# Kernel tuning notes

Measured on AMD Instinct MI355X. Metric: run time of the kernel, lower is better.

Reference implementation:

```python
import jax, jax.numpy as jnp
import numpy as np
from jax import lax

DT = 0.01        # self.dt
DT_SCALE = 1.0   # forward default


def _christoffel(v, x, U, W):
    # Low-rank quadratic Christoffel contraction (U, W as in verlet_fused):
    # gamma = (tanh(x @ U) * (v @ U)^2) @ W        [B, D]
    h = v @ U                 # [B, R]
    gate = jnp.tanh(x @ U)    # [B, R]
    return (gate * h * h) @ W


def setup_inputs() -> dict:
    key = jax.random.key(0)
    ks = jax.random.split(key, 5)
    B, D, R = 4096, 1024, 256
    x = jax.random.normal(ks[0], (B, D), dtype=jnp.float32)
    v = jax.random.normal(ks[1], (B, D), dtype=jnp.float32)
    force = jax.random.normal(ks[2], (B, D), dtype=jnp.float32)
    U = jax.random.normal(ks[3], (D, R), dtype=jnp.float32) * (D ** -0.5)
    W = jax.random.normal(ks[4], (R, D), dtype=jnp.float32) * (R ** -0.5)
    return {"x": x, "v": v, "force": force, "U": U, "W": W, "steps": 8}


def reference(x, v, force, U, W, steps):
    dt = jnp.float32(DT * DT_SCALE)
    half = jnp.float32(0.5)

    def step(carry, _):
        x, v = carry
        a = force - _christoffel(v, x, U, W)
        v_half = v + half * dt * a
        x = x + dt * v_half
        a_next = force - _christoffel(v_half, x, U, W)
        v = v_half + half * dt * a_next
        return (x, v), None

    (x, v), _ = lax.scan(step, (x, v), None, length=steps)
    return (x, v)
```

## Files before the change

kernel.cpp:

```cpp
#include <hip/hip_runtime.h>

typedef __bf16 bf16_t;
typedef __bf16 bf16x2 __attribute__((ext_vector_type(2)));
typedef __bf16 bf16x8 __attribute__((ext_vector_type(8)));
typedef float f32x4 __attribute__((ext_vector_type(4)));

#define MFMA_BF16(a, b, c) __builtin_amdgcn_mfma_f32_16x16x32_bf16((a), (b), (c), 0, 0, 0)

static constexpr int Bn = 4096;
static constexpr int Dn = 1024;
static constexpr int Rn = 256;
static constexpr int BT = 16;
static constexpr float DTv = 0.01f;
static constexpr float HDT = 0.005f;

__device__ __forceinline__ int swz(int col) { return col ^ (((col >> 5) & 7) << 2); }

__global__ __launch_bounds__(1024)
void setup_kernel(const float* __restrict__ U, const float* __restrict__ W,
                  bf16_t* __restrict__ Upk, bf16_t* __restrict__ Wpk,
                  bf16_t* __restrict__ WUpk) {
  __shared__ __align__(16) bf16_t wbuf[16 * 1032];
  const int tid = (int)threadIdx.x;
  const int b = (int)blockIdx.x;
  if (b < 32) {
    int t = b * 1024 + tid;
    int l = t & 63, f = t >> 6;
    int kb = f & 31, ct = f >> 5;
    int row0 = kb * 32 + (l >> 4) * 8, col = ct * 16 + (l & 15);
    bf16x8 v;
#pragma unroll
    for (int j = 0; j < 8; ++j) v[j] = (bf16_t)U[(size_t)(row0 + j) * Rn + col];
    ((bf16x8*)Upk)[t] = v;
  } else if (b < 64) {
    int t = (b - 32) * 1024 + tid;
    int l = t & 63, f = t >> 6;
    int kb = f & 7, ct = f >> 3;
    int row0 = kb * 32 + (l >> 4) * 8, col = ct * 16 + (l & 15);
    bf16x8 v;
#pragma unroll
    for (int j = 0; j < 8; ++j) v[j] = (bf16_t)W[(size_t)(row0 + j) * Dn + col];
    ((bf16x8*)Wpk)[t] = v;
  } else {
    const int m = b - 64;
    const int wv = tid >> 6;
    const int l = tid & 63;
    const int ln = l & 15;
    const int quad = l >> 4;
    {
      int row = tid >> 6;
      int c0 = (tid & 63) * 16;
      const float* src = W + (size_t)(m * 16 + row) * Dn + c0;
      bf16_t* dst = wbuf + row * 1032 + c0;
#pragma unroll
      for (int j = 0; j < 16; ++j) dst[j] = (bf16_t)src[j];
    }
    __syncthreads();
    const int ucol = wv * 16 + ln;
    float uf[8][8];
#pragma unroll
    for (int p = 0; p < 8; ++p)
#pragma unroll
      for (int j = 0; j < 8; ++j)
        uf[p][j] = U[(size_t)(p * 32 + quad * 8 + j) * Rn + ucol];
    f32x4 acc = {0.f, 0.f, 0.f, 0.f};
    const bf16_t* arow = wbuf + ln * 1032 + quad * 8;
#pragma unroll
    for (int kb = 0; kb < 32; ++kb) {
      bf16x8 bb;
#pragma unroll
      for (int j = 0; j < 8; ++j) bb[j] = (bf16_t)uf[kb & 7][j];
      const bf16x8 a = *(const bf16x8*)(arow + kb * 32);
      acc = MFMA_BF16(a, bb, acc);
      if (kb < 24) {
#pragma unroll
        for (int j = 0; j < 8; ++j)
          uf[kb & 7][j] = U[(size_t)((kb + 8) * 32 + quad * 8 + j) * Rn + ucol];
      }
    }
#pragma unroll
    for (int r = 0; r < 4; ++r) {
      int rw = m * 16 + quad * 4 + r;
      int kb = rw >> 5;
      int sub = (rw >> 3) & 3;
      int j = rw & 7;
      size_t slot = ((size_t)(wv * 8 + kb) * 64 + sub * 16 + ln) * 8 + j;
      WUpk[slot] = (bf16_t)acc[r];
    }
  }
}

__global__ __launch_bounds__(1024)
__attribute__((amdgpu_waves_per_eu(4, 4)))
void integrate_kernel(const float* __restrict__ x_in, const float* __restrict__ v_in,
                      const float* __restrict__ force,
                      const bf16_t* __restrict__ Upk, const bf16_t* __restrict__ Wpk,
                      const bf16_t* __restrict__ WUpk,
                      const int* __restrict__ steps_p, float* __restrict__ out) {
  __shared__ __align__(16) char smem[49920];
  bf16_t* abuf = (bf16_t*)smem;
  float* fsb = (float*)smem;

  const int tid = (int)threadIdx.x;
  const int wv = tid >> 6;
  const int l = tid & 63;
  const int ln = l & 15;
  const int quad = l >> 4;
  const int s = steps_p[0];
  const int nhalf = 2 * s;
  const int row_base = (int)blockIdx.x * BT;

  float* out_x = out;
  float* out_v = out + (size_t)Bn * Dn;

  const int frow = tid >> 7;
  const int fr = (tid & 127) * 8;
  const int sc0 = swz(fr);
  const int sc1 = sc0 ^ 4;
  int csw[4];
#pragma unroll
  for (int i = 0; i < 4; ++i) csw[i] = swz((wv * 4 + i) * 16 + ln);

  float xs[4][4], vs[4][4];
  bf16x2 fs2[4][2];

  auto load_chunk = [&](const float* __restrict__ srcA, int HF, auto sink) {
    const float* src_ = srcA + (size_t)(row_base + HF * 8) * Dn;
    f32x4 a_ = *(const f32x4*)(src_ + tid * 8);
    f32x4 b_ = *(const f32x4*)(src_ + tid * 8 + 4);
    *(f32x4*)(fsb + frow * 1024 + sc0) = a_;
    *(f32x4*)(fsb + frow * 1024 + sc1) = b_;
    __syncthreads();
    if ((quad >> 1) == HF) {
#pragma unroll
      for (int i = 0; i < 4; ++i)
#pragma unroll
        for (int r = 0; r < 4; ++r)
          sink(i, r, fsb[((quad & 1) * 4 + r) * 1024 + csw[i]]);
    }
    __syncthreads();
  };
  load_chunk(x_in, 0, [&](int i, int r, float v_) { xs[i][r] = v_; });
  load_chunk(x_in, 1, [&](int i, int r, float v_) { xs[i][r] = v_; });
  load_chunk(v_in, 0, [&](int i, int r, float v_) { vs[i][r] = v_; });
  load_chunk(v_in, 1, [&](int i, int r, float v_) { vs[i][r] = v_; });
  load_chunk(force, 0, [&](int i, int r, float v_) { fs2[i][r >> 1][r & 1] = (bf16_t)v_; });
  load_chunk(force, 1, [&](int i, int r, float v_) { fs2[i][r >> 1][r & 1] = (bf16_t)v_; });

  f32x4 hx = {0.f, 0.f, 0.f, 0.f};
  f32x4 hv = {0.f, 0.f, 0.f, 0.f};
  f32x4 FU = {0.f, 0.f, 0.f, 0.f};
#pragma unroll
  for (int kh = 0; kh < 2; ++kh) {
    if ((wv >> 3) == kh) {
#pragma unroll
      for (int i = 0; i < 4; ++i) {
        const int col = (wv * 4 + i) * 16 + ln - kh * 512;
#pragma unroll
        for (int r = 0; r < 4; ++r) {
          const int ro = (quad * 4 + r) * 520 + col;
          abuf[ro] = (bf16_t)xs[i][r];
          abuf[8320 + ro] = (bf16_t)vs[i][r];
          abuf[16640 + ro] = fs2[i][r >> 1][r & 1];
        }
      }
    }
    __syncthreads();
    const bf16x8* up = (const bf16x8*)Upk + ((size_t)wv * 32 + kh * 16) * 64 + l;
    const bf16_t* ax = abuf + ln * 520 + quad * 8;
    bf16x8 ur[8];
#pragma unroll
    for (int p = 0; p < 8; ++p) ur[p] = up[p * 64];
#pragma unroll
    for (int kb = 0; kb < 16; ++kb) {
      const bf16x8 b = ur[kb & 7];
      if (kb < 8) ur[kb & 7] = up[(kb + 8) * 64];
      const bf16x8 a0 = *(const bf16x8*)(ax + kb * 32);
      const bf16x8 a1 = *(const bf16x8*)(ax + 8320 + kb * 32);
      const bf16x8 a2 = *(const bf16x8*)(ax + 16640 + kb * 32);
      hx = MFMA_BF16(a0, b, hx);
      hv = MFMA_BF16(a1, b, hv);
      FU = MFMA_BF16(a2, b, FU);
    }
    __syncthreads();
  }

  bf16x8 wu[8];
  {
    const bf16x8* wub = (const bf16x8*)WUpk + (size_t)wv * 8 * 64 + l;
#pragma unroll
    for (int kb = 0; kb < 8; ++kb) wu[kb] = wub[kb * 64];
  }

  f32x4 S1 = {0.f, 0.f, 0.f, 0.f};
  f32x4 S2 = {0.f, 0.f, 0.f, 0.f};
  bf16_t* tbase = (bf16_t*)smem;
  for (int h = 0; h < nhalf; ++h) {
    if (h & 1) {
#pragma unroll
      for (int r = 0; r < 4; ++r) hx[r] += DTv * hv[r];
    }
    const float ch = (float)(s - ((h + 1) >> 1));
    bf16_t* tb = tbase + (h & 1) * 4224;
#pragma unroll
    for (int r = 0; r < 4; ++r) {
      float a = fminf(fmaxf(hx[r], -15.f), 15.f);
      const float e = __expf(2.f * a);
      const float gate = (e - 1.f) / (e + 1.f);
      const float t = gate * hv[r] * hv[r];
      S1[r] += t;
      S2[r] += ch * t;
      tb[(quad * 4 + r) * 264 + wv * 16 + ln] = (bf16_t)t;
    }
    __syncthreads();
    f32x4 g0 = {0.f, 0.f, 0.f, 0.f};
    f32x4 g1 = {0.f, 0.f, 0.f, 0.f};
    const bf16_t* trow = tb + ln * 264 + quad * 8;
#pragma unroll
    for (int kb = 0; kb < 8; kb += 2) {
      g0 = MFMA_BF16(*(const bf16x8*)(trow + kb * 32), wu[kb], g0);
      g1 = MFMA_BF16(*(const bf16x8*)(trow + (kb + 1) * 32), wu[kb + 1], g1);
    }
#pragma unroll
    for (int r = 0; r < 4; ++r) hv[r] += HDT * (FU[r] - (g0[r] + g1[r]));
  }
  __syncthreads();

  bf16_t* sbuf = (bf16_t*)smem;
#pragma unroll
  for (int r = 0; r < 4; ++r) {
    const int ro = (quad * 4 + r) * 264 + wv * 16 + ln;
    sbuf[ro] = (bf16_t)S1[r];
    sbuf[4224 + ro] = (bf16_t)S2[r];
  }
  __syncthreads();
  f32x4 ac1[4], ac2[4];
#pragma unroll
  for (int i = 0; i < 4; ++i) {
    ac1[i] = (f32x4){0.f, 0.f, 0.f, 0.f};
    ac2[i] = (f32x4){0.f, 0.f, 0.f, 0.f};
  }
  {
    const bf16x8* wp = (const bf16x8*)Wpk + (size_t)(wv * 4) * 8 * 64 + l;
    const bf16_t* s1row = sbuf + ln * 264 + quad * 8;
    const bf16_t* s2row = s1row + 4224;
    bf16x8 wr[4];
#pragma unroll
    for (int i = 0; i < 4; ++i) wr[i] = wp[i * 8 * 64];
#pragma unroll
    for (int kb = 0; kb < 8; ++kb) {
      const bf16x8 a1 = *(const bf16x8*)(s1row + kb * 32);
      const bf16x8 a2 = *(const bf16x8*)(s2row + kb * 32);
#pragma unroll
      for (int i = 0; i < 4; ++i) {
        const bf16x8 b = wr[i];
        if (kb < 7) wr[i] = wp[i * 8 * 64 + (kb + 1) * 64];
        ac1[i] = MFMA_BF16(a1, b, ac1[i]);
        ac2[i] = MFMA_BF16(a2, b, ac2[i]);
      }
    }
  }
  __syncthreads();

  const float sf = (float)s;
  const float c_vf = sf * DTv;
  const float c_xf = sf * sf * DTv * HDT;
  auto store_chunk = [&](float* __restrict__ dstA, int HF, auto vex) {
    if ((quad >> 1) == HF) {
#pragma unroll
      for (int i = 0; i < 4; ++i)
#pragma unroll
        for (int r = 0; r < 4; ++r)
          fsb[((quad & 1) * 4 + r) * 1024 + csw[i]] = vex(i, r);
    }
    __syncthreads();
    float* dst_ = dstA + (size_t)(row_base + HF * 8) * Dn;
    *(f32x4*)(dst_ + tid * 8) = *(const f32x4*)(fsb + frow * 1024 + sc0);
    *(f32x4*)(dst_ + tid * 8 + 4) = *(const f32x4*)(fsb + frow * 1024 + sc1);
    __syncthreads();
  };
  auto vval = [&](int i, int r) {
    return vs[i][r] + c_vf * (float)fs2[i][r >> 1][r & 1] - HDT * ac1[i][r];
  };
  auto xval = [&](int i, int r) {
    return xs[i][r] + c_vf * vs[i][r] + c_xf * (float)fs2[i][r >> 1][r & 1] -
           DTv * HDT * ac2[i][r];
  };
  store_chunk(out_v, 0, vval);
  store_chunk(out_v, 1, vval);
  store_chunk(out_x, 0, xval);
  store_chunk(out_x, 1, xval);
}

extern "C" void kernel_launch(void* const* d_in, const int* in_sizes, int n_in,
                              void* d_out, int out_size, void* d_ws, size_t ws_size,
                              hipStream_t stream) {
  const float* x = (const float*)d_in[0];
  const float* v = (const float*)d_in[1];
  const float* force = (const float*)d_in[2];
  const float* U = (const float*)d_in[3];
  const float* W = (const float*)d_in[4];
  const int* steps = (const int*)d_in[5];

  bf16_t* Upk = (bf16_t*)d_ws;
  bf16_t* Wpk = (bf16_t*)((char*)d_ws + 512 * 1024);
  bf16_t* WUpk = (bf16_t*)((char*)d_ws + 1024 * 1024);

  setup_kernel<<<80, 1024, 0, stream>>>(U, W, Upk, Wpk, WUpk);
  integrate_kernel<<<Bn / BT, 1024, 0, stream>>>(x, v, force, Upk, Wpk, WUpk, steps,
                                                 (float*)d_out);
}
```

Measured before the change: 159.9 us.

## Prefetch all input chunks up front, deepen W prefetch, split MFMA accumulators

Issues all six global loads for x, v and force before any LDS restaging, so the memory latency of the loads overlaps instead of being serialized behind barriers. Global access now uses contiguous 4-float strides per thread for coalescing. The final W GEMM prefetches two k-blocks ahead, and the per-step Christoffel MFMA chain uses four independent accumulators instead of two to shorten dependency chains. These changes raise register pressure, since 12 extra f32x4 values and more W buffers are held live.

```diff
diff --git a/kernel.cpp b/kernel.cpp
--- a/kernel.cpp
+++ b/kernel.cpp
@@ -113,10 +113,6 @@
   float* out_x = out;
   float* out_v = out + (size_t)Bn * Dn;
 
-  const int frow = tid >> 7;
-  const int fr = (tid & 127) * 8;
-  const int sc0 = swz(fr);
-  const int sc1 = sc0 ^ 4;
   int csw[4];
 #pragma unroll
   for (int i = 0; i < 4; ++i) csw[i] = swz((wv * 4 + i) * 16 + ln);
@@ -124,12 +120,25 @@
   float xs[4][4], vs[4][4];
   bf16x2 fs2[4][2];
 
-  auto load_chunk = [&](const float* __restrict__ srcA, int HF, auto sink) {
-    const float* src_ = srcA + (size_t)(row_base + HF * 8) * Dn;
-    f32x4 a_ = *(const f32x4*)(src_ + tid * 8);
-    f32x4 b_ = *(const f32x4*)(src_ + tid * 8 + 4);
-    *(f32x4*)(fsb + frow * 1024 + sc0) = a_;
-    *(f32x4*)(fsb + frow * 1024 + sc1) = b_;
+  f32x4 ldv[3][2][2];
+  {
+    const float* bases[3] = {x_in, v_in, force};
+#pragma unroll
+    for (int a = 0; a < 3; ++a)
+#pragma unroll
+      for (int HF = 0; HF < 2; ++HF) {
+        const float* src_ = bases[a] + (size_t)(row_base + HF * 8) * Dn + tid * 4;
+        ldv[a][HF][0] = *(const f32x4*)src_;
+        ldv[a][HF][1] = *(const f32x4*)(src_ + 4096);
+      }
+  }
+
+  auto restage = [&](const f32x4* lv, int HF, auto sink) {
+#pragma unroll
+    for (int k = 0; k < 2; ++k) {
+      const int fi = k * 4096 + tid * 4;
+      *(f32x4*)(fsb + (fi >> 10) * 1024 + swz(fi & 1023)) = lv[k];
+    }
     __syncthreads();
     if ((quad >> 1) == HF) {
 #pragma unroll
@@ -140,12 +149,12 @@
     }
     __syncthreads();
   };
-  load_chunk(x_in, 0, [&](int i, int r, float v_) { xs[i][r] = v_; });
-  load_chunk(x_in, 1, [&](int i, int r, float v_) { xs[i][r] = v_; });
-  load_chunk(v_in, 0, [&](int i, int r, float v_) { vs[i][r] = v_; });
-  load_chunk(v_in, 1, [&](int i, int r, float v_) { vs[i][r] = v_; });
-  load_chunk(force, 0, [&](int i, int r, float v_) { fs2[i][r >> 1][r & 1] = (bf16_t)v_; });
-  load_chunk(force, 1, [&](int i, int r, float v_) { fs2[i][r >> 1][r & 1] = (bf16_t)v_; });
+  restage(ldv[0][0], 0, [&](int i, int r, float v_) { xs[i][r] = v_; });
+  restage(ldv[0][1], 1, [&](int i, int r, float v_) { xs[i][r] = v_; });
+  restage(ldv[1][0], 0, [&](int i, int r, float v_) { vs[i][r] = v_; });
+  restage(ldv[1][1], 1, [&](int i, int r, float v_) { vs[i][r] = v_; });
+  restage(ldv[2][0], 0, [&](int i, int r, float v_) { fs2[i][r >> 1][r & 1] = (bf16_t)v_; });
+  restage(ldv[2][1], 1, [&](int i, int r, float v_) { fs2[i][r >> 1][r & 1] = (bf16_t)v_; });
 
   f32x4 hx = {0.f, 0.f, 0.f, 0.f};
   f32x4 hv = {0.f, 0.f, 0.f, 0.f};
@@ -215,14 +224,20 @@
     __syncthreads();
     f32x4 g0 = {0.f, 0.f, 0.f, 0.f};
     f32x4 g1 = {0.f, 0.f, 0.f, 0.f};
+    f32x4 g2 = {0.f, 0.f, 0.f, 0.f};
+    f32x4 g3 = {0.f, 0.f, 0.f, 0.f};
     const bf16_t* trow = tb + ln * 264 + quad * 8;
-#pragma unroll
-    for (int kb = 0; kb < 8; kb += 2) {
-      g0 = MFMA_BF16(*(const bf16x8*)(trow + kb * 32), wu[kb], g0);
-      g1 = MFMA_BF16(*(const bf16x8*)(trow + (kb + 1) * 32), wu[kb + 1], g1);
-    }
-#pragma unroll
-    for (int r = 0; r < 4; ++r) hv[r] += HDT * (FU[r] - (g0[r] + g1[r]));
+    g0 = MFMA_BF16(*(const bf16x8*)(trow + 0 * 32), wu[0], g0);
+    g1 = MFMA_BF16(*(const bf16x8*)(trow + 1 * 32), wu[1], g1);
+    g2 = MFMA_BF16(*(const bf16x8*)(trow + 2 * 32), wu[2], g2);
+    g3 = MFMA_BF16(*(const bf16x8*)(trow + 3 * 32), wu[3], g3);
+    g0 = MFMA_BF16(*(const bf16x8*)(trow + 4 * 32), wu[4], g0);
+    g1 = MFMA_BF16(*(const bf16x8*)(trow + 5 * 32), wu[5], g1);
+    g2 = MFMA_BF16(*(const bf16x8*)(trow + 6 * 32), wu[6], g2);
+    g3 = MFMA_BF16(*(const bf16x8*)(trow + 7 * 32), wu[7], g3);
+#pragma unroll
+    for (int r = 0; r < 4; ++r)
+      hv[r] += HDT * (FU[r] - ((g0[r] + g1[r]) + (g2[r] + g3[r])));
   }
   __syncthreads();
 
@@ -244,17 +259,20 @@
     const bf16x8* wp = (const bf16x8*)Wpk + (size_t)(wv * 4) * 8 * 64 + l;
     const bf16_t* s1row = sbuf + ln * 264 + quad * 8;
     const bf16_t* s2row = s1row + 4224;
-    bf16x8 wr[4];
-#pragma unroll
-    for (int i = 0; i < 4; ++i) wr[i] = wp[i * 8 * 64];
+    bf16x8 wr[4][2];
+#pragma unroll
+    for (int i = 0; i < 4; ++i) {
+      wr[i][0] = wp[i * 512];
+      wr[i][1] = wp[i * 512 + 64];
+    }
 #pragma unroll
     for (int kb = 0; kb < 8; ++kb) {
       const bf16x8 a1 = *(const bf16x8*)(s1row + kb * 32);
       const bf16x8 a2 = *(const bf16x8*)(s2row + kb * 32);
 #pragma unroll
       for (int i = 0; i < 4; ++i) {
-        const bf16x8 b = wr[i];
-        if (kb < 7) wr[i] = wp[i * 8 * 64 + (kb + 1) * 64];
+        const bf16x8 b = wr[i][kb & 1];
+        if (kb < 6) wr[i][kb & 1] = wp[i * 512 + (kb + 2) * 64];
         ac1[i] = MFMA_BF16(a1, b, ac1[i]);
         ac2[i] = MFMA_BF16(a2, b, ac2[i]);
       }
@@ -275,8 +293,11 @@
     }
     __syncthreads();
     float* dst_ = dstA + (size_t)(row_base + HF * 8) * Dn;
-    *(f32x4*)(dst_ + tid * 8) = *(const f32x4*)(fsb + frow * 1024 + sc0);
-    *(f32x4*)(dst_ + tid * 8 + 4) = *(const f32x4*)(fsb + frow * 1024 + sc1);
+#pragma unroll
+    for (int k = 0; k < 2; ++k) {
+      const int fi = k * 4096 + tid * 4;
+      *(f32x4*)(dst_ + fi) = *(const f32x4*)(fsb + (fi >> 10) * 1024 + swz(fi & 1023));
+    }
     __syncthreads();
   };
   auto vval = [&](int i, int r) {
```

Result: slower. 164.7 us (+3.0%).
